# Optimization experiments

Measured on AMD Instinct MI355X. Metric: run time of the kernel, lower is better.

The kernel has to match this reference:

```python
import jax, jax.numpy as jnp
import numpy as np

B, L, D = 2, 1024, 1024
H = 16
NL = 2
DFF = 4 * D
EPS = 1e-5
W_SCALE = 0.02


def rmsnorm(x, w):
    # x * rsqrt(mean(x^2, -1) + eps) * w   (computed in fp32 as in the torch code)
    xf = x.astype(jnp.float32)
    n = xf * jax.lax.rsqrt(jnp.mean(xf * xf, axis=-1, keepdims=True) + EPS)
    return n.astype(x.dtype) * w


def setup_inputs() -> dict:
    key = jax.random.key(0)
    ks = jax.random.split(key, 10)
    x = jax.random.normal(ks[0], (B, L, D), dtype=jnp.float32)
    # torch nn.Linear weight layout: [out_features, in_features]; y = x @ W.T + b
    qw = jax.random.normal(ks[1], (NL, D, D), dtype=jnp.float32) * W_SCALE
    kw = jax.random.normal(ks[2], (NL, D, D), dtype=jnp.float32) * W_SCALE
    vw = jax.random.normal(ks[3], (NL, D, D), dtype=jnp.float32) * W_SCALE
    ow = jax.random.normal(ks[4], (NL, D, D), dtype=jnp.float32) * W_SCALE
    pn_w = jnp.ones((NL, D), dtype=jnp.float32)
    ln_w = jnp.ones((NL, D), dtype=jnp.float32)
    fc_w = jax.random.normal(ks[5], (NL, DFF, D), dtype=jnp.float32) * W_SCALE
    fc2_w = jax.random.normal(ks[6], (NL, D, DFF), dtype=jnp.float32) * W_SCALE
    fc2_b = jnp.zeros((NL, D), dtype=jnp.float32)
    return {"x": x, "qw": qw, "kw": kw, "vw": vw, "ow": ow,
            "pn_w": pn_w, "ln_w": ln_w, "fc_w": fc_w, "fc2_w": fc2_w, "fc2_b": fc2_b}


def reference(x, qw, kw, vw, ow, pn_w, ln_w, fc_w, fc2_w, fc2_b):
    d = D // H
    for i in range(NL):
        # --- LinearAttention block (dropout=0 -> identity) ---
        h = rmsnorm(x, pn_w[i])                                   # [B,L,D]
        Q = (h @ qw[i].T).reshape(B, L, H, d)
        K = (h @ kw[i].T).reshape(B, L, H, d)
        V = (h @ vw[i].T).reshape(B, L, H, d)
        # outer-product state per position, cumulated over L (causal linear attn)
        W = jnp.einsum('blhd,blhe->blhde', K, V)                  # [B,L,H,d,d]
        W = jnp.cumsum(W, axis=1)
        a = jnp.einsum('blhd,blhde->blhe', Q, W).reshape(B, L, D)
        x = x + a @ ow[i].T
        # --- MLP block ---
        m = rmsnorm(x, ln_w[i])
        f = jax.nn.gelu(m @ fc_w[i].T, approximate=False)         # torch nn.GELU default = exact
        x = x + f @ fc2_w[i].T + fc2_b[i]
    return x
```

## Files before the change

kernel.cpp:

```cpp
#include <hip/hip_runtime.h>

#define BB 2
#define LL 1024
#define DD 1024
#define HH 16
#define HD 64
#define DFFN 4096
#define MM (BB*LL)
#define QS 3072

using u16 = unsigned short;
typedef __bf16 bf16x8 __attribute__((ext_vector_type(8)));
typedef float f32x4 __attribute__((ext_vector_type(4)));

__device__ __forceinline__ float b2f(u16 u) {
  union { unsigned int i; float f; } v; v.i = ((unsigned int)u) << 16; return v.f;
}
__device__ __forceinline__ u16 f2b(float f) {
  union { float f; unsigned int i; } v; v.f = f;
  unsigned int x = v.i;
  return (u16)((x + 0x7fffu + ((x >> 16) & 1u)) >> 16);
}
__device__ __forceinline__ float gelu_exact(float x) {
  return 0.5f * x * (1.0f + erff(x * 0.70710678118654752f));
}
__device__ __forceinline__ void gl2lds16(const void* g, void* l) {
  __builtin_amdgcn_global_load_lds((const __attribute__((address_space(1))) void*)g,
                                   (__attribute__((address_space(3))) void*)l, 16, 0, 0);
}

template<int N>
__device__ __forceinline__ void s_wait_vm() {
  if constexpr (N == 0)       asm volatile("s_waitcnt vmcnt(0) lgkmcnt(0)" ::: "memory");
  else if constexpr (N == 3)  asm volatile("s_waitcnt vmcnt(3) lgkmcnt(0)" ::: "memory");
  else if constexpr (N == 4)  asm volatile("s_waitcnt vmcnt(4) lgkmcnt(0)" ::: "memory");
  else if constexpr (N == 6)  asm volatile("s_waitcnt vmcnt(6) lgkmcnt(0)" ::: "memory");
  else if constexpr (N == 8)  asm volatile("s_waitcnt vmcnt(8) lgkmcnt(0)" ::: "memory");
  else if constexpr (N == 12) asm volatile("s_waitcnt vmcnt(12) lgkmcnt(0)" ::: "memory");
  __builtin_amdgcn_sched_barrier(0);
}

__device__ __forceinline__ void xcd_remap(int& bx, int& by, int& bz) {
  const int gx = gridDim.x, gy = gridDim.y;
  const int nb = gx * gy * gridDim.z;
  int b = blockIdx.x + gx * (blockIdx.y + gy * blockIdx.z);
  if ((nb & 127) == 0) {
    const int xcd = b & 7, seq = b >> 3;
    b = (((seq >> 4) << 3) + xcd) * 16 + (seq & 15);
  }
  bx = b % gx; const int rest = b / gx;
  by = rest % gy; bz = rest / gy;
}

__global__ __launch_bounds__(256) void castw_kernel(const float* __restrict__ in,
                                                    u16* __restrict__ out, int n8) {
  int i = blockIdx.x * 256 + threadIdx.x;
  if (i >= n8) return;
  const float4 a = reinterpret_cast<const float4*>(in)[2 * i];
  const float4 b = reinterpret_cast<const float4*>(in)[2 * i + 1];
  uint4 o;
  o.x = (unsigned)f2b(a.x) | ((unsigned)f2b(a.y) << 16);
  o.y = (unsigned)f2b(a.z) | ((unsigned)f2b(a.w) << 16);
  o.z = (unsigned)f2b(b.x) | ((unsigned)f2b(b.y) << 16);
  o.w = (unsigned)f2b(b.z) | ((unsigned)f2b(b.w) << 16);
  reinterpret_cast<uint4*>(out)[i] = o;
}
__global__ __launch_bounds__(256) void castw3_kernel(const float* __restrict__ s0,
                                                     const float* __restrict__ s1,
                                                     const float* __restrict__ s2,
                                                     u16* __restrict__ out, int n8) {
  int i = blockIdx.x * 256 + threadIdx.x;
  if (i >= n8) return;
  const float* in = (blockIdx.y == 0) ? s0 : (blockIdx.y == 1) ? s1 : s2;
  u16* dst = out + (size_t)blockIdx.y * n8 * 8;
  const float4 a = reinterpret_cast<const float4*>(in)[2 * i];
  const float4 b = reinterpret_cast<const float4*>(in)[2 * i + 1];
  uint4 o;
  o.x = (unsigned)f2b(a.x) | ((unsigned)f2b(a.y) << 16);
  o.y = (unsigned)f2b(a.z) | ((unsigned)f2b(a.w) << 16);
  o.z = (unsigned)f2b(b.x) | ((unsigned)f2b(b.y) << 16);
  o.w = (unsigned)f2b(b.z) | ((unsigned)f2b(b.w) << 16);
  reinterpret_cast<uint4*>(dst)[i] = o;
}

__global__ __launch_bounds__(256) void init_out_kernel(float* __restrict__ out,
                                                       const float* __restrict__ resid,
                                                       const float* __restrict__ bias) {
  const int i = blockIdx.x * 256 + threadIdx.x;
  float4 v = reinterpret_cast<const float4*>(resid)[i];
  if (bias != nullptr) {
    const float4 bv = *reinterpret_cast<const float4*>(bias + ((i * 4) & (DD - 1)));
    v.x += bv.x; v.y += bv.y; v.z += bv.z; v.w += bv.w;
  }
  reinterpret_cast<float4*>(out)[i] = v;
}

__global__ __launch_bounds__(256) void rmsnorm_kernel(const float* __restrict__ x,
                                                      const float* __restrict__ w,
                                                      u16* __restrict__ out) {
  const int row = blockIdx.x, t = threadIdx.x;
  const float4 v = reinterpret_cast<const float4*>(x + (size_t)row * DD)[t];
  float ss = v.x*v.x + v.y*v.y + v.z*v.z + v.w*v.w;
  #pragma unroll
  for (int o = 32; o > 0; o >>= 1) ss += __shfl_down(ss, o);
  __shared__ float red[4];
  if ((t & 63) == 0) red[t >> 6] = ss;
  __syncthreads();
  const float inv = rsqrtf((red[0] + red[1] + red[2] + red[3]) * (1.0f / DD) + 1e-5f);
  const float4 wv = reinterpret_cast<const float4*>(w)[t];
  ushort4 o;
  o.x = f2b(v.x * inv * wv.x);
  o.y = f2b(v.y * inv * wv.y);
  o.z = f2b(v.z * inv * wv.z);
  o.w = f2b(v.w * inv * wv.w);
  reinterpret_cast<ushort4*>(out + (size_t)row * DD)[t] = o;
}

template<int ROWS, int NT>
__device__ __forceinline__ void dma32(const u16* __restrict__ g, int r0, int K, int kt,
                                      int t, u16* lds) {
  #pragma unroll
  for (int i = 0; i < ROWS * 4 / NT; i++) {
    const int c = i * NT + t;
    const int row = (c & 7) | ((c >> 5) << 3);
    const int kc = (c >> 3) & 3;
    gl2lds16(g + (size_t)(r0 + row) * K + kt + kc * 8, &lds[c * 8]);
  }
}
__device__ __forceinline__ const bf16x8* lds_frag(const u16* base, int r, int fq) {
  const int p = (r & 7) | (fq << 3) | ((r >> 3) << 5);
  return reinterpret_cast<const bf16x8*>(&base[p * 8]);
}
__device__ __forceinline__ void mfma_tile32(const u16* Asb, const u16* Bsb,
                                            int wm, int wn, int fr, int fq, f32x4 acc[4][4]) {
  bf16x8 af[4], bfv[4];
  #pragma unroll
  for (int i = 0; i < 4; i++) af[i] = *lds_frag(Asb, wm + i * 16 + fr, fq);
  #pragma unroll
  for (int j = 0; j < 4; j++) bfv[j] = *lds_frag(Bsb, wn + j * 16 + fr, fq);
  #pragma unroll
  for (int i = 0; i < 4; i++)
    #pragma unroll
    for (int j = 0; j < 4; j++)
      acc[i][j] = __builtin_amdgcn_mfma_f32_16x16x32_bf16(af[i], bfv[j], acc[i][j], 0, 0, 0);
}

template<int BM, int BN>
__device__ __forceinline__ void gemm_pipeline(const u16* __restrict__ A,
                                              const u16* __restrict__ Wb,
                                              int K, int k0, int nt, int m0, int n0,
                                              u16* As, u16* Bs, int t,
                                              int wm, int wn, int fr, int fq,
                                              f32x4 acc[4][4]) {
  constexpr int NT = (BM / 64) * (BN / 64) * 64;
  constexpr int L = (BM + BN) * 4 / NT;
  #pragma unroll
  for (int s = 0; s < 3; ++s) {
    dma32<BM, NT>(A, m0, K, k0 + s * 32, t, As + s * BM * 32);
    dma32<BN, NT>(Wb, n0, K, k0 + s * 32, t, Bs + s * BN * 32);
  }
  int pb = 0;
  for (int tt = 0; tt < nt; ++tt) {
    const int ahead = nt - 1 - tt;
    if (ahead >= 2)      s_wait_vm<2 * L>();
    else if (ahead == 1) s_wait_vm<L>();
    else                 s_wait_vm<0>();
    __builtin_amdgcn_s_barrier();
    __builtin_amdgcn_sched_barrier(0);
    if (tt + 3 < nt) {
      int p3 = pb + 3; if (p3 >= 4) p3 -= 4;
      dma32<BM, NT>(A, m0, K, k0 + (tt + 3) * 32, t, As + p3 * BM * 32);
      dma32<BN, NT>(Wb, n0, K, k0 + (tt + 3) * 32, t, Bs + p3 * BN * 32);
      __builtin_amdgcn_sched_barrier(0);
    }
    mfma_tile32(As + pb * BM * 32, Bs + pb * BN * 32, wm, wn, fr, fq, acc);
    pb = (pb + 1) & 3;
  }
}

template<int BM, int BN, int ACT>
__global__ __launch_bounds__((BM/64)*(BN/64)*64)
void mfma_gemm(const u16* __restrict__ A, const u16* __restrict__ Wb,
               u16* __restrict__ Cb, int N, int K) {
  constexpr int WCOLS = BN / 64;
  __shared__ u16 As[4 * BM * 32];
  __shared__ u16 Bs[4 * BN * 32];
  int bx, by, bz;
  xcd_remap(bx, by, bz);
  const int t = threadIdx.x;
  const int lane = t & 63, w = t >> 6;
  const int wm = (w / WCOLS) * 64, wn = (w % WCOLS) * 64;
  const int m0 = by * BM, n0 = bx * BN;
  const int fr = lane & 15, fq = lane >> 4;

  f32x4 acc[4][4] = {};
  gemm_pipeline<BM, BN>(A, Wb, K, 0, K / 32, m0, n0, As, Bs, t, wm, wn, fr, fq, acc);

  #pragma unroll
  for (int i = 0; i < 4; i++)
    #pragma unroll
    for (int j = 0; j < 4; j++)
      #pragma unroll
      for (int r = 0; r < 4; r++) {
        const int row = m0 + wm + i * 16 + fq * 4 + r;
        const int col = n0 + wn + j * 16 + fr;
        float val = acc[i][j][r];
        if (ACT == 1) val = gelu_exact(val);
        Cb[(size_t)row * N + col] = f2b(val);
      }
}

template<int BM, int BN, int SPLIT>
__global__ __launch_bounds__((BM/64)*(BN/64)*64)
void mfma_gemm_sk(const u16* __restrict__ A, const u16* __restrict__ Wb,
                  float* __restrict__ Co, int N, int K) {
  constexpr int WCOLS = BN / 64;
  __shared__ u16 As[4 * BM * 32];
  __shared__ u16 Bs[4 * BN * 32];
  int bx, by, bz;
  xcd_remap(bx, by, bz);
  const int t = threadIdx.x;
  const int lane = t & 63, w = t >> 6;
  const int wm = (w / WCOLS) * 64, wn = (w % WCOLS) * 64;
  const int m0 = by * BM, n0 = bx * BN;
  const int fr = lane & 15, fq = lane >> 4;
  const int Kc = K / SPLIT, k0 = bz * Kc;

  f32x4 acc[4][4] = {};
  gemm_pipeline<BM, BN>(A, Wb, K, k0, Kc / 32, m0, n0, As, Bs, t, wm, wn, fr, fq, acc);

  #pragma unroll
  for (int i = 0; i < 4; i++)
    #pragma unroll
    for (int j = 0; j < 4; j++)
      #pragma unroll
      for (int r = 0; r < 4; r++) {
        const int row = m0 + wm + i * 16 + fq * 4 + r;
        const int col = n0 + wn + j * 16 + fr;
        unsafeAtomicAdd(&Co[(size_t)row * N + col], acc[i][j][r]);
      }
}

__global__ __launch_bounds__(256) void kv_trans(const u16* __restrict__ QKV,
                                                u16* __restrict__ Kt, u16* __restrict__ Vt) {
  __shared__ u16 T[64][72];
  const int tile = blockIdx.x;
  const int h2 = blockIdx.y;
  const int b = blockIdx.z;
  const int h = h2 & 15, which = h2 >> 4;
  const int t = threadIdx.x;
  const int pos = t >> 2, d0 = (t & 3) * 16;
  const u16* src = QKV + ((size_t)(b * LL) + tile * 64 + pos) * QS + 1024 + which * 1024 + h * HD + d0;
  union { uint4 u[2]; u16 s[16]; } pk;
  pk.u[0] = reinterpret_cast<const uint4*>(src)[0];
  pk.u[1] = reinterpret_cast<const uint4*>(src)[1];
  #pragma unroll
  for (int j = 0; j < 16; j++) T[d0 + j][pos] = pk.s[j];
  __syncthreads();
  const int d = t >> 2, p0 = (t & 3) * 16;
  u16* dst = (which ? Vt : Kt) + ((size_t)(b * HH + h) * HD + d) * LL + tile * 64 + p0;
  union { uint4 u[2]; u16 s[16]; } ok;
  #pragma unroll
  for (int j = 0; j < 16; j++) ok.s[j] = T[d][p0 + j];
  reinterpret_cast<uint4*>(dst)[0] = ok.u[0];
  reinterpret_cast<uint4*>(dst)[1] = ok.u[1];
}

__global__ __launch_bounds__(256) void attn_phase1(const u16* __restrict__ QKV,
                                                   const u16* __restrict__ Kt,
                                                   const u16* __restrict__ Vt,
                                                   u16* __restrict__ Oa,
                                                   u16* __restrict__ Slt) {
  __shared__ u16 Ss[4][16][64];
  const int tile = blockIdx.x, h = blockIdx.y, b = blockIdx.z;
  const int t = threadIdx.x, lane = t & 63, w = t >> 6;
  const int fr = lane & 15, fq = lane >> 4;
  const size_t tok0 = (size_t)(b * LL + tile * 64);
  const size_t bh = (size_t)(b * HH + h);
  const u16* Qb  = QKV + tok0 * QS + h * HD;
  const u16* Kb  = Qb + 1024;
  const u16* Ktb = Kt + bh * (HD * LL) + tile * 64;
  const u16* Vtb = Vt + bh * (HD * LL) + tile * 64;

  bf16x8 aq[2], bk[4][2];
  #pragma unroll
  for (int kh = 0; kh < 2; kh++)
    aq[kh] = *reinterpret_cast<const bf16x8*>(Qb + (size_t)(16*w + fr) * QS + kh*32 + fq*8);
  #pragma unroll
  for (int n4 = 0; n4 < 4; n4++)
    #pragma unroll
    for (int kh = 0; kh < 2; kh++)
      bk[n4][kh] = *reinterpret_cast<const bf16x8*>(Kb + (size_t)(16*n4 + fr) * QS + kh*32 + fq*8);
  f32x4 sacc[4] = {};
  #pragma unroll
  for (int n4 = 0; n4 < 4; n4++) {
    sacc[n4] = __builtin_amdgcn_mfma_f32_16x16x32_bf16(aq[0], bk[n4][0], sacc[n4], 0, 0, 0);
    sacc[n4] = __builtin_amdgcn_mfma_f32_16x16x32_bf16(aq[1], bk[n4][1], sacc[n4], 0, 0, 0);
  }
  #pragma unroll
  for (int n4 = 0; n4 < 4; n4++)
    #pragma unroll
    for (int r = 0; r < 4; r++) {
      const bool keep = (16*w + 4*fq + r) >= (16*n4 + fr);
      Ss[w][4*fq + r][16*n4 + fr] = keep ? f2b(sacc[n4][r]) : (u16)0;
    }
  __syncthreads();

  bf16x8 va[2], kt[4][2];
  #pragma unroll
  for (int kh = 0; kh < 2; kh++)
    va[kh] = *reinterpret_cast<const bf16x8*>(Vtb + (size_t)(16*w + fr) * LL + kh*32 + fq*8);
  #pragma unroll
  for (int n4 = 0; n4 < 4; n4++)
    #pragma unroll
    for (int kh = 0; kh < 2; kh++)
      kt[n4][kh] = *reinterpret_cast<const bf16x8*>(Ktb + (size_t)(16*n4 + fr) * LL + kh*32 + fq*8);
  f32x4 lacc[4] = {};
  #pragma unroll
  for (int n4 = 0; n4 < 4; n4++) {
    lacc[n4] = __builtin_amdgcn_mfma_f32_16x16x32_bf16(va[0], kt[n4][0], lacc[n4], 0, 0, 0);
    lacc[n4] = __builtin_amdgcn_mfma_f32_16x16x32_bf16(va[1], kt[n4][1], lacc[n4], 0, 0, 0);
  }
  u16* So = Slt + (bh * 16 + tile) * 4096;
  #pragma unroll
  for (int n4 = 0; n4 < 4; n4++)
    #pragma unroll
    for (int r = 0; r < 4; r++)
      So[(size_t)(16*w + 4*fq + r) * 64 + 16*n4 + fr] = f2b(lacc[n4][r]);

  bf16x8 sa[2], vb[4][2];
  #pragma unroll
  for (int kh = 0; kh < 2; kh++)
    sa[kh] = *reinterpret_cast<const bf16x8*>(&Ss[w][fr][kh*32 + fq*8]);
  #pragma unroll
  for (int n4 = 0; n4 < 4; n4++)
    #pragma unroll
    for (int kh = 0; kh < 2; kh++)
      vb[n4][kh] = *reinterpret_cast<const bf16x8*>(Vtb + (size_t)(16*n4 + fr) * LL + kh*32 + fq*8);
  f32x4 oacc[4] = {};
  #pragma unroll
  for (int n4 = 0; n4 < 4; n4++) {
    oacc[n4] = __builtin_amdgcn_mfma_f32_16x16x32_bf16(sa[0], vb[n4][0], oacc[n4], 0, 0, 0);
    oacc[n4] = __builtin_amdgcn_mfma_f32_16x16x32_bf16(sa[1], vb[n4][1], oacc[n4], 0, 0, 0);
  }
  u16* Ob = Oa + (tok0 + 16*w) * DD + h * HD;
  #pragma unroll
  for (int n4 = 0; n4 < 4; n4++)
    #pragma unroll
    for (int r = 0; r < 4; r++)
      Ob[(size_t)(4*fq + r) * DD + 16*n4 + fr] = f2b(oacc[n4][r]);
}

__global__ __launch_bounds__(256) void attn_phase2(const u16* __restrict__ Slt,
                                                   u16* __restrict__ Wc) {
  const int rg = blockIdx.x, h = blockIdx.y, b = blockIdx.z;
  const size_t base = ((size_t)((b * HH + h) * 16)) * 4096 + rg * 512 + threadIdx.x * 2;
  float r0 = 0.f, r1 = 0.f;
  for (int tl = 0; tl < 16; tl++) {
    const size_t p = base + (size_t)tl * 4096;
    const unsigned d = *reinterpret_cast<const unsigned*>(Slt + p);
    *reinterpret_cast<unsigned*>(Wc + p) = (unsigned)f2b(r0) | ((unsigned)f2b(r1) << 16);
    r0 += b2f((u16)(d & 0xffff));
    r1 += b2f((u16)(d >> 16));
  }
}

__global__ __launch_bounds__(256) void attn_phase3(const u16* __restrict__ QKV,
                                                   const u16* __restrict__ Wc,
                                                   u16* __restrict__ Oa) {
  const int tile = blockIdx.x, h = blockIdx.y, b = blockIdx.z;
  const int t = threadIdx.x, lane = t & 63, w = t >> 6;
  const int fr = lane & 15, fq = lane >> 4;
  const size_t tok0 = (size_t)(b * LL + tile * 64);
  const size_t bh = (size_t)(b * HH + h);
  const u16* Qb = QKV + tok0 * QS + h * HD;
  const u16* Wb = Wc + (bh * 16 + tile) * 4096;

  bf16x8 aq[2], wb[4][2];
  #pragma unroll
  for (int kh = 0; kh < 2; kh++)
    aq[kh] = *reinterpret_cast<const bf16x8*>(Qb + (size_t)(16*w + fr) * QS + kh*32 + fq*8);
  #pragma unroll
  for (int n4 = 0; n4 < 4; n4++)
    #pragma unroll
    for (int kh = 0; kh < 2; kh++)
      wb[n4][kh] = *reinterpret_cast<const bf16x8*>(Wb + (size_t)(16*n4 + fr) * 64 + kh*32 + fq*8);
  f32x4 oacc[4] = {};
  #pragma unroll
  for (int n4 = 0; n4 < 4; n4++) {
    oacc[n4] = __builtin_amdgcn_mfma_f32_16x16x32_bf16(aq[0], wb[n4][0], oacc[n4], 0, 0, 0);
    oacc[n4] = __builtin_amdgcn_mfma_f32_16x16x32_bf16(aq[1], wb[n4][1], oacc[n4], 0, 0, 0);
  }
  u16* Ob = Oa + (tok0 + 16*w) * DD + h * HD;
  #pragma unroll
  for (int n4 = 0; n4 < 4; n4++)
    #pragma unroll
    for (int r = 0; r < 4; r++) {
      const size_t idx = (size_t)(4*fq + r) * DD + 16*n4 + fr;
      Ob[idx] = f2b(b2f(Ob[idx]) + oacc[n4][r]);
    }
}

extern "C" void kernel_launch(void* const* d_in, const int* in_sizes, int n_in,
                              void* d_out, int out_size, void* d_ws, size_t ws_size,
                              hipStream_t stream) {
  const float* x_in = (const float*)d_in[0];
  const float* qw   = (const float*)d_in[1];
  const float* kw   = (const float*)d_in[2];
  const float* vw   = (const float*)d_in[3];
  const float* ow   = (const float*)d_in[4];
  const float* pn   = (const float*)d_in[5];
  const float* ln   = (const float*)d_in[6];
  const float* fcw  = (const float*)d_in[7];
  const float* fc2w = (const float*)d_in[8];
  const float* fc2b = (const float*)d_in[9];

  char* ws = (char*)d_ws;
  u16* wbuf = (u16*)ws;
  u16* slt  = (u16*)ws;
  u16* wcum = (u16*)(ws + (size_t)(4 << 20));
  u16* h    = (u16*)(ws + (size_t)(8 << 20));
  u16* qkv  = (u16*)(ws + (size_t)(12 << 20));
  u16* f    = (u16*)(ws + (size_t)(12 << 20));
  u16* vt   = (u16*)(ws + (size_t)(24 << 20));
  u16* kt   = (u16*)(ws + (size_t)(28 << 20));
  float* xf = (float*)d_out;

  const int n8D = DD * DD / 8;
  const int n8F = DFFN * DD / 8;
  const int gInit = MM * DD / 4 / 256;

  for (int i = 0; i < 2; i++) {
    const float* qwi  = qw   + (size_t)i * DD * DD;
    const float* kwi  = kw   + (size_t)i * DD * DD;
    const float* vwi  = vw   + (size_t)i * DD * DD;
    const float* owi  = ow   + (size_t)i * DD * DD;
    const float* fcwi = fcw  + (size_t)i * DFFN * DD;
    const float* f2wi = fc2w + (size_t)i * DD * DFFN;
    const float* src  = (i == 0) ? x_in : xf;

    rmsnorm_kernel<<<MM, 256, 0, stream>>>(src, pn + i * DD, h);
    castw3_kernel<<<dim3(n8D / 256, 3), 256, 0, stream>>>(qwi, kwi, vwi, wbuf, n8D);
    mfma_gemm<256, 128, 0><<<dim3(QS / 128, MM / 256), 512, 0, stream>>>(
        h, wbuf, qkv, QS, DD);
    kv_trans<<<dim3(16, 32, BB), 256, 0, stream>>>(qkv, kt, vt);
    attn_phase1<<<dim3(16, HH, BB), 256, 0, stream>>>(qkv, kt, vt, h, slt);
    attn_phase2<<<dim3(8, HH, BB), 256, 0, stream>>>(slt, wcum);
    attn_phase3<<<dim3(16, HH, BB), 256, 0, stream>>>(qkv, wcum, h);
    castw_kernel<<<n8D / 256, 256, 0, stream>>>(owi, wbuf, n8D);
    init_out_kernel<<<gInit, 256, 0, stream>>>(xf, src, nullptr);
    mfma_gemm_sk<256, 128, 4><<<dim3(DD / 128, MM / 256, 4), 512, 0, stream>>>(
        h, wbuf, xf, DD, DD);
    rmsnorm_kernel<<<MM, 256, 0, stream>>>(xf, ln + i * DD, h);
    castw_kernel<<<n8F / 256, 256, 0, stream>>>(fcwi, wbuf, n8F);
    mfma_gemm<256, 128, 1><<<dim3(DFFN / 128, MM / 256), 512, 0, stream>>>(
        h, wbuf, f, DFFN, DD);
    castw_kernel<<<n8F / 256, 256, 0, stream>>>(f2wi, wbuf, n8F);
    float* co = (i == 1) ? (float*)d_out : xf;
    init_out_kernel<<<gInit, 256, 0, stream>>>(co, xf, fc2b + i * DD);
    mfma_gemm_sk<256, 128, 4><<<dim3(DD / 128, MM / 256, 4), 512, 0, stream>>>(
        f, wbuf, co, DD, DFFN);
  }
}
```

Baseline: 623.0 us.

## Split GEMM k-step into two MFMA phases with interleaved DMA and priority

```diff
diff --git a/kernel.cpp b/kernel.cpp
--- a/kernel.cpp
+++ b/kernel.cpp
@@ -31,12 +31,9 @@
 
 template<int N>
 __device__ __forceinline__ void s_wait_vm() {
-  if constexpr (N == 0)       asm volatile("s_waitcnt vmcnt(0) lgkmcnt(0)" ::: "memory");
-  else if constexpr (N == 3)  asm volatile("s_waitcnt vmcnt(3) lgkmcnt(0)" ::: "memory");
-  else if constexpr (N == 4)  asm volatile("s_waitcnt vmcnt(4) lgkmcnt(0)" ::: "memory");
-  else if constexpr (N == 6)  asm volatile("s_waitcnt vmcnt(6) lgkmcnt(0)" ::: "memory");
-  else if constexpr (N == 8)  asm volatile("s_waitcnt vmcnt(8) lgkmcnt(0)" ::: "memory");
-  else if constexpr (N == 12) asm volatile("s_waitcnt vmcnt(12) lgkmcnt(0)" ::: "memory");
+  if constexpr (N == 0)       asm volatile("s_waitcnt vmcnt(0)" ::: "memory");
+  else if constexpr (N == 3)  asm volatile("s_waitcnt vmcnt(3)" ::: "memory");
+  else if constexpr (N == 6)  asm volatile("s_waitcnt vmcnt(6)" ::: "memory");
   __builtin_amdgcn_sched_barrier(0);
 }
 
@@ -131,49 +128,78 @@
   const int p = (r & 7) | (fq << 3) | ((r >> 3) << 5);
   return reinterpret_cast<const bf16x8*>(&base[p * 8]);
 }
-__device__ __forceinline__ void mfma_tile32(const u16* Asb, const u16* Bsb,
-                                            int wm, int wn, int fr, int fq, f32x4 acc[4][4]) {
-  bf16x8 af[4], bfv[4];
-  #pragma unroll
-  for (int i = 0; i < 4; i++) af[i] = *lds_frag(Asb, wm + i * 16 + fr, fq);
-  #pragma unroll
-  for (int j = 0; j < 4; j++) bfv[j] = *lds_frag(Bsb, wn + j * 16 + fr, fq);
-  #pragma unroll
-  for (int i = 0; i < 4; i++)
-    #pragma unroll
-    for (int j = 0; j < 4; j++)
-      acc[i][j] = __builtin_amdgcn_mfma_f32_16x16x32_bf16(af[i], bfv[j], acc[i][j], 0, 0, 0);
-}
+
+#define MFMA_BF16 __builtin_amdgcn_mfma_f32_16x16x32_bf16
 
 template<int BM, int BN>
-__device__ __forceinline__ void gemm_pipeline(const u16* __restrict__ A,
-                                              const u16* __restrict__ Wb,
-                                              int K, int k0, int nt, int m0, int n0,
-                                              u16* As, u16* Bs, int t,
-                                              int wm, int wn, int fr, int fq,
-                                              f32x4 acc[4][4]) {
+__device__ __forceinline__ void gemm_pipe(const u16* __restrict__ A,
+                                          const u16* __restrict__ Wb,
+                                          int K, int k0, int nt, int m0, int n0,
+                                          u16* As, u16* Bs, int t,
+                                          int wm, int wn, int fr, int fq,
+                                          f32x4 acc[4][4]) {
   constexpr int NT = (BM / 64) * (BN / 64) * 64;
-  constexpr int L = (BM + BN) * 4 / NT;
   #pragma unroll
   for (int s = 0; s < 3; ++s) {
     dma32<BM, NT>(A, m0, K, k0 + s * 32, t, As + s * BM * 32);
     dma32<BN, NT>(Wb, n0, K, k0 + s * 32, t, Bs + s * BN * 32);
   }
+  s_wait_vm<6>();
+  __builtin_amdgcn_s_barrier();
   int pb = 0;
   for (int tt = 0; tt < nt; ++tt) {
-    const int ahead = nt - 1 - tt;
-    if (ahead >= 2)      s_wait_vm<2 * L>();
-    else if (ahead == 1) s_wait_vm<L>();
-    else                 s_wait_vm<0>();
+    const u16* Asb = As + pb * BM * 32;
+    const u16* Bsb = Bs + pb * BN * 32;
+    const int p3 = (pb + 3) & 3;
+    const bool st = (tt + 3 < nt);
+    bf16x8 a0 = *lds_frag(Asb, wm + 0 * 16 + fr, fq);
+    bf16x8 a1 = *lds_frag(Asb, wm + 1 * 16 + fr, fq);
+    bf16x8 b0 = *lds_frag(Bsb, wn + 0 * 16 + fr, fq);
+    bf16x8 b1 = *lds_frag(Bsb, wn + 1 * 16 + fr, fq);
+    bf16x8 b2 = *lds_frag(Bsb, wn + 2 * 16 + fr, fq);
+    bf16x8 b3 = *lds_frag(Bsb, wn + 3 * 16 + fr, fq);
+    if (st) dma32<BM, NT>(A, m0, K, k0 + (tt + 3) * 32, t, As + p3 * BM * 32);
+    __builtin_amdgcn_sched_barrier(0);
     __builtin_amdgcn_s_barrier();
-    __builtin_amdgcn_sched_barrier(0);
-    if (tt + 3 < nt) {
-      int p3 = pb + 3; if (p3 >= 4) p3 -= 4;
-      dma32<BM, NT>(A, m0, K, k0 + (tt + 3) * 32, t, As + p3 * BM * 32);
-      dma32<BN, NT>(Wb, n0, K, k0 + (tt + 3) * 32, t, Bs + p3 * BN * 32);
-      __builtin_amdgcn_sched_barrier(0);
+    asm volatile("s_waitcnt lgkmcnt(0)" ::: "memory");
+    __builtin_amdgcn_sched_barrier(0);
+    __builtin_amdgcn_s_setprio(1);
+    acc[0][0] = MFMA_BF16(a0, b0, acc[0][0], 0, 0, 0);
+    acc[0][1] = MFMA_BF16(a0, b1, acc[0][1], 0, 0, 0);
+    acc[0][2] = MFMA_BF16(a0, b2, acc[0][2], 0, 0, 0);
+    acc[0][3] = MFMA_BF16(a0, b3, acc[0][3], 0, 0, 0);
+    acc[1][0] = MFMA_BF16(a1, b0, acc[1][0], 0, 0, 0);
+    acc[1][1] = MFMA_BF16(a1, b1, acc[1][1], 0, 0, 0);
+    acc[1][2] = MFMA_BF16(a1, b2, acc[1][2], 0, 0, 0);
+    acc[1][3] = MFMA_BF16(a1, b3, acc[1][3], 0, 0, 0);
+    __builtin_amdgcn_s_setprio(0);
+    __builtin_amdgcn_sched_barrier(0);
+    __builtin_amdgcn_s_barrier();
+    bf16x8 a2 = *lds_frag(Asb, wm + 2 * 16 + fr, fq);
+    bf16x8 a3 = *lds_frag(Asb, wm + 3 * 16 + fr, fq);
+    if (st) dma32<BN, NT>(Wb, n0, K, k0 + (tt + 3) * 32, t, Bs + p3 * BN * 32);
+    __builtin_amdgcn_sched_barrier(0);
+    __builtin_amdgcn_s_barrier();
+    asm volatile("s_waitcnt lgkmcnt(0)" ::: "memory");
+    __builtin_amdgcn_sched_barrier(0);
+    __builtin_amdgcn_s_setprio(1);
+    acc[2][0] = MFMA_BF16(a2, b0, acc[2][0], 0, 0, 0);
+    acc[2][1] = MFMA_BF16(a2, b1, acc[2][1], 0, 0, 0);
+    acc[2][2] = MFMA_BF16(a2, b2, acc[2][2], 0, 0, 0);
+    acc[2][3] = MFMA_BF16(a2, b3, acc[2][3], 0, 0, 0);
+    acc[3][0] = MFMA_BF16(a3, b0, acc[3][0], 0, 0, 0);
+    acc[3][1] = MFMA_BF16(a3, b1, acc[3][1], 0, 0, 0);
+    acc[3][2] = MFMA_BF16(a3, b2, acc[3][2], 0, 0, 0);
+    acc[3][3] = MFMA_BF16(a3, b3, acc[3][3], 0, 0, 0);
+    __builtin_amdgcn_s_setprio(0);
+    __builtin_amdgcn_sched_barrier(0);
+    if (tt + 1 < nt) {
+      const int rem = nt - 2 - tt;
+      if (rem >= 2)      s_wait_vm<6>();
+      else if (rem == 1) s_wait_vm<3>();
+      else               s_wait_vm<0>();
+      __builtin_amdgcn_s_barrier();
     }
-    mfma_tile32(As + pb * BM * 32, Bs + pb * BN * 32, wm, wn, fr, fq, acc);
     pb = (pb + 1) & 3;
   }
 }
@@ -194,7 +220,7 @@
   const int fr = lane & 15, fq = lane >> 4;
 
   f32x4 acc[4][4] = {};
-  gemm_pipeline<BM, BN>(A, Wb, K, 0, K / 32, m0, n0, As, Bs, t, wm, wn, fr, fq, acc);
+  gemm_pipe<BM, BN>(A, Wb, K, 0, K / 32, m0, n0, As, Bs, t, wm, wn, fr, fq, acc);
 
   #pragma unroll
   for (int i = 0; i < 4; i++)
@@ -227,7 +253,7 @@
   const int Kc = K / SPLIT, k0 = bz * Kc;
 
   f32x4 acc[4][4] = {};
-  gemm_pipeline<BM, BN>(A, Wb, K, k0, Kc / 32, m0, n0, As, Bs, t, wm, wn, fr, fq, acc);
+  gemm_pipe<BM, BN>(A, Wb, K, k0, Kc / 32, m0, n0, As, Bs, t, wm, wn, fr, fq, acc);
 
   #pragma unroll
   for (int i = 0; i < 4; i++)
@@ -294,8 +320,8 @@
   f32x4 sacc[4] = {};
   #pragma unroll
   for (int n4 = 0; n4 < 4; n4++) {
-    sacc[n4] = __builtin_amdgcn_mfma_f32_16x16x32_bf16(aq[0], bk[n4][0], sacc[n4], 0, 0, 0);
-    sacc[n4] = __builtin_amdgcn_mfma_f32_16x16x32_bf16(aq[1], bk[n4][1], sacc[n4], 0, 0, 0);
+    sacc[n4] = MFMA_BF16(aq[0], bk[n4][0], sacc[n4], 0, 0, 0);
+    sacc[n4] = MFMA_BF16(aq[1], bk[n4][1], sacc[n4], 0, 0, 0);
   }
   #pragma unroll
   for (int n4 = 0; n4 < 4; n4++)
@@ -318,8 +344,8 @@
   f32x4 lacc[4] = {};
   #pragma unroll
   for (int n4 = 0; n4 < 4; n4++) {
-    lacc[n4] = __builtin_amdgcn_mfma_f32_16x16x32_bf16(va[0], kt[n4][0], lacc[n4], 0, 0, 0);
-    lacc[n4] = __builtin_amdgcn_mfma_f32_16x16x32_bf16(va[1], kt[n4][1], lacc[n4], 0, 0, 0);
+    lacc[n4] = MFMA_BF16(va[0], kt[n4][0], lacc[n4], 0, 0, 0);
+    lacc[n4] = MFMA_BF16(va[1], kt[n4][1], lacc[n4], 0, 0, 0);
   }
   u16* So = Slt + (bh * 16 + tile) * 4096;
   #pragma unroll
@@ -340,8 +366,8 @@
   f32x4 oacc[4] = {};
   #pragma unroll
   for (int n4 = 0; n4 < 4; n4++) {
-    oacc[n4] = __builtin_amdgcn_mfma_f32_16x16x32_bf16(sa[0], vb[n4][0], oacc[n4], 0, 0, 0);
-    oacc[n4] = __builtin_amdgcn_mfma_f32_16x16x32_bf16(sa[1], vb[n4][1], oacc[n4], 0, 0, 0);
+    oacc[n4] = MFMA_BF16(sa[0], vb[n4][0], oacc[n4], 0, 0, 0);
+    oacc[n4] = MFMA_BF16(sa[1], vb[n4][1], oacc[n4], 0, 0, 0);
   }
   u16* Ob = Oa + (tok0 + 16*w) * DD + h * HD;
   #pragma unroll
@@ -388,8 +414,8 @@
   f32x4 oacc[4] = {};
   #pragma unroll
   for (int n4 = 0; n4 < 4; n4++) {
-    oacc[n4] = __builtin_amdgcn_mfma_f32_16x16x32_bf16(aq[0], wb[n4][0], oacc[n4], 0, 0, 0);
-    oacc[n4] = __builtin_amdgcn_mfma_f32_16x16x32_bf16(aq[1], wb[n4][1], oacc[n4], 0, 0, 0);
+    oacc[n4] = MFMA_BF16(aq[0], wb[n4][0], oacc[n4], 0, 0, 0);
+    oacc[n4] = MFMA_BF16(aq[1], wb[n4][1], oacc[n4], 0, 0, 0);
   }
   u16* Ob = Oa + (tok0 + 16*w) * DD + h * HD;
   #pragma unroll
```

Measured after the change: 581.5 us. 1.07x faster.
